# Kernel optimization log

Hardware: AMD Instinct MI355X
Metric: run time of the kernel (lower is better)

## Reference

```python
import jax, jax.numpy as jnp
import numpy as np

N = 4_000_000   # number of sparse voxels
H = 128         # parent-grid extent per axis (input coords < 256 -> parents < 128)


def setup_inputs() -> dict:
    key = jax.random.key(0)
    # col 0 = batch index, cols 1:4 = integer xyz voxel coords in [0, 256)
    coords = jax.random.randint(key, (N, 4), 0, 256, dtype=jnp.int32)
    # spnn.Conv3d(1,1,k=2) kernel: (2^3, in=1, out=1), constant-init to 1.0
    kernel = jnp.ones((8, 1, 1), dtype=jnp.float32)
    return {"coords": coords, "kernel": kernel}


def _fog(coords, kernel):
    b = coords[:, 0].astype(jnp.int64)
    xyz = coords[:, 1:]
    # pos(): 3-bit occupancy code from LSBs of xyz, feat = 2^code
    bits = xyz & 1                                        # (N, 3)
    pos = bits[:, 0] + 2 * bits[:, 1] + 4 * bits[:, 2]    # (N,) in [0, 8)
    feats = (jnp.int32(1) << pos).astype(jnp.float32)     # (N,) values {1,...,128}

    # 2x2x2 stride-2 sparse conv with all-ones kernel == sum over the 8 children
    # of each parent voxel. The child's kernel-offset index is exactly `pos`.
    pxyz = (xyz >> 1).astype(jnp.int64)                   # parent coords
    pkey = ((b * H + pxyz[:, 0]) * H + pxyz[:, 1]) * H + pxyz[:, 2]

    ukeys, inv = jnp.unique(pkey, size=N, fill_value=-1, return_inverse=True)
    inv = inv.ravel()

    contrib = feats * kernel[pos, 0, 0]                   # all-ones kernel -> feats
    out_feats = jax.ops.segment_sum(contrib, inv, num_segments=N)  # (N,)

    # decode unique parent keys back to (batch, x, y, z); pad slots -> -1
    valid = ukeys >= 0
    k = jnp.where(valid, ukeys, 0)
    oz = k % H
    k = k // H
    oy = k % H
    k = k // H
    ox = k % H
    ob = k // H
    out_coords = jnp.stack([ob, ox, oy, oz], axis=-1).astype(jnp.int32)
    out_coords = jnp.where(valid[:, None], out_coords, jnp.int32(-1))
    return out_coords, out_feats


def reference(coords, kernel):
    return _fog(coords, kernel)
```

## Files before the change

### kernel.cpp

```cpp
#include <hip/hip_runtime.h>

#define NB_BITS     11
#define N_BUCKETS   (1 << NB_BITS)
#define LOCAL_BITS  18
#define LOCAL_WORDS 8192
#define LKMASK      ((1u << LOCAL_BITS) - 1u)
#define KEYMASK     0x1FFFFFFFu
#define NXCD        8
#define WCAP        512
#define WSHIFT      9
#define FE_CAP      2560
#define PPT         8
#define TILE        (1024 * PPT)

__device__ __forceinline__ unsigned make_key(int4 c) {
    return ((((unsigned)c.x << 7) | (unsigned)(c.y >> 1)) << 7 | (unsigned)(c.z >> 1)) << 7
         | (unsigned)(c.w >> 1);
}

template<int NW>
__device__ inline void block_scan(unsigned v, unsigned* wsum, unsigned& excl, unsigned& total) {
    int t = threadIdx.x, ln = t & 63, wv = t >> 6;
    unsigned incl = v;
    #pragma unroll
    for (int off = 1; off < 64; off <<= 1) {
        unsigned y = __shfl_up(incl, off, 64);
        if (ln >= off) incl += y;
    }
    if (ln == 63) wsum[wv] = incl;
    __syncthreads();
    if (wv == 0) {
        unsigned s = (ln < NW) ? wsum[ln] : 0u;
        #pragma unroll
        for (int off = 1; off < NW; off <<= 1) {
            unsigned y = __shfl_up(s, off, 64);
            if (ln >= off) s += y;
        }
        if (ln < NW) wsum[ln] = s;
    }
    __syncthreads();
    excl = (wv ? wsum[wv - 1] : 0u) + incl - v;
    total = wsum[NW - 1];
}

__device__ __forceinline__ void gb_setup(const unsigned* gcur, int b, unsigned* gb) {
    int t = threadIdx.x;
    unsigned gv = 0;
    if (t < 8) gv = min(gcur[(unsigned)t * N_BUCKETS + (unsigned)b], (unsigned)WCAP);
    if (t < 64) {
        unsigned incl = gv;
        #pragma unroll
        for (int off = 1; off < 8; off <<= 1) {
            unsigned y = __shfl_up(incl, off, 64);
            if (t >= off) incl += y;
        }
        if (t < 8) gb[t + 1] = incl;
        if (t == 0) gb[0] = 0u;
    }
}

__global__ void __launch_bounds__(1024, 8)
build_pass(const int4* __restrict__ coords,
           unsigned* __restrict__ gcur,
           unsigned* __restrict__ pairs,
           int n) {
    __shared__ unsigned h[N_BUCKETS];
    int t = threadIdx.x, blk = blockIdx.x;
    unsigned xcd = (unsigned)blk & 7u;
    int base = blk * TILE;
    unsigned skey[PPT], lrank[PPT];
    h[t] = 0u; h[t + 1024] = 0u;
    #pragma unroll
    for (int m = 0; m < PPT; ++m) {
        int i = base + t + m * 1024;
        if (i < n) {
            int4 c = coords[i];
            unsigned key = make_key(c);
            unsigned pos = (unsigned)((c.y & 1) | ((c.z & 1) << 1) | ((c.w & 1) << 2));
            skey[m] = (pos << 29) | key;
        }
    }
    __syncthreads();
    #pragma unroll
    for (int m = 0; m < PPT; ++m) {
        int i = base + t + m * 1024;
        if (i < n)
            lrank[m] = atomicAdd(&h[(skey[m] & KEYMASK) >> LOCAL_BITS], 1u);
    }
    __syncthreads();
    #pragma unroll
    for (int q = 0; q < 2; ++q) {
        int j = t + q * 1024;
        unsigned c = h[j];
        if (c) h[j] = atomicAdd(&gcur[xcd * N_BUCKETS + (unsigned)j], c);
    }
    __syncthreads();
    #pragma unroll
    for (int m = 0; m < PPT; ++m) {
        int i = base + t + m * 1024;
        if (i < n) {
            unsigned b = (skey[m] & KEYMASK) >> LOCAL_BITS;
            unsigned o = h[b] + lrank[m];
            if (o < WCAP)
                pairs[(((b << 3) | xcd) << WSHIFT) + o] = skey[m];
        }
    }
}

__global__ void __launch_bounds__(512, 8)
count_pass(const unsigned* __restrict__ pairs,
           const unsigned* __restrict__ gcur,
           unsigned* __restrict__ ucount) {
    __shared__ unsigned bm[LOCAL_WORDS];
    __shared__ unsigned wsum[8];
    __shared__ unsigned gb[NXCD + 1];
    int t = threadIdx.x, b = blockIdx.x;
    gb_setup(gcur, b, gb);
    #pragma unroll
    for (int m = 0; m < 4; ++m)
        ((uint4*)bm)[t + 512 * m] = make_uint4(0u, 0u, 0u, 0u);
    __syncthreads();
    unsigned tot = gb[NXCD];
    for (unsigned p = (unsigned)t; p < tot; p += 512u) {
        unsigned g = 0;
        #pragma unroll
        for (int j = 1; j < NXCD; ++j) g += (p >= gb[j]) ? 1u : 0u;
        unsigned lk = pairs[((((unsigned)b << 3) | g) << WSHIFT) + (p - gb[g])] & LKMASK;
        atomicOr(&bm[lk >> 5], 1u << (lk & 31u));
    }
    __syncthreads();
    unsigned v = 0;
    #pragma unroll
    for (int m = 0; m < 16; ++m) v += __popc(bm[t + 512 * m]);
    int ln = t & 63;
    #pragma unroll
    for (int off = 1; off < 64; off <<= 1) v += __shfl_xor(v, off, 64);
    if (ln == 0) wsum[t >> 6] = v;
    __syncthreads();
    if (t == 0) {
        unsigned c = 0;
        #pragma unroll
        for (int m = 0; m < 8; ++m) c += wsum[m];
        ucount[b] = c;
    }
}

__global__ void __launch_bounds__(1024, 8)
emit_pass(const unsigned* __restrict__ pairs,
          const unsigned* __restrict__ gcur,
          const unsigned* __restrict__ ucount,
          const float* __restrict__ kern,
          float4* __restrict__ out_coords,
          float* __restrict__ out_feats, int n) {
    __shared__ unsigned       bm[LOCAL_WORDS];
    __shared__ unsigned short pfx[LOCAL_WORDS];
    __shared__ float          fe[FE_CAP];
    __shared__ unsigned wsum[16];
    __shared__ unsigned gb[NXCD + 1];
    __shared__ unsigned ubS, totS;
    __shared__ float    kl[8];
    int t = threadIdx.x, b = blockIdx.x;
    if (t < 8) kl[t] = (float)(1 << t) * kern[t];
    gb_setup(gcur, b, gb);
    ((uint4*)bm)[t] = make_uint4(0u, 0u, 0u, 0u);
    ((uint4*)bm)[t + 1024] = make_uint4(0u, 0u, 0u, 0u);
    for (int i = t; i < FE_CAP; i += 1024) fe[i] = 0.f;
    __syncthreads();
    unsigned tot = gb[NXCD];
    unsigned pk[5];
    if (t >= 64) {
        #pragma unroll
        for (int k = 0; k < 5; ++k) {
            unsigned p = (unsigned)(t - 64) + (unsigned)k * 960u;
            if (p < tot) {
                unsigned g = 0;
                #pragma unroll
                for (int j = 1; j < NXCD; ++j) g += (p >= gb[j]) ? 1u : 0u;
                unsigned v = pairs[((((unsigned)b << 3) | g) << WSHIFT) + (p - gb[g])];
                pk[k] = v;
                unsigned lk = v & LKMASK;
                atomicOr(&bm[lk >> 5], 1u << (lk & 31u));
            }
        }
    } else {
        int ln = t;
        unsigned sum = 0;
        const uint4* uc4 = (const uint4*)ucount;
        #pragma unroll
        for (int q = 0; q < 8; ++q) {
            uint4 u = uc4[ln * 8 + q];
            sum += u.x + u.y + u.z + u.w;
        }
        unsigned incl = sum;
        #pragma unroll
        for (int off = 1; off < 64; off <<= 1) {
            unsigned y = __shfl_up(incl, off, 64);
            if (ln >= off) incl += y;
        }
        if (ln == 63) totS = incl;
        unsigned exclv = incl - sum;
        if (ln == (b >> 5)) {
            unsigned r = exclv;
            int lim = b & 31;
            for (int m = 0; m < lim; ++m) r += ucount[(b & ~31) + m];
            ubS = r;
        }
    }
    __syncthreads();
    uint4 q0 = ((uint4*)bm)[2 * t], q1 = ((uint4*)bm)[2 * t + 1];
    unsigned pc[8] = { (unsigned)__popc(q0.x), (unsigned)__popc(q0.y),
                       (unsigned)__popc(q0.z), (unsigned)__popc(q0.w),
                       (unsigned)__popc(q1.x), (unsigned)__popc(q1.y),
                       (unsigned)__popc(q1.z), (unsigned)__popc(q1.w) };
    unsigned psum = 0;
    #pragma unroll
    for (int m = 0; m < 8; ++m) psum += pc[m];
    unsigned excl, cnt;
    block_scan<16>(psum, wsum, excl, cnt);
    {
        unsigned run = excl, pw[4];
        #pragma unroll
        for (int m = 0; m < 4; ++m) {
            unsigned lo = run & 0xFFFFu; run += pc[2 * m];
            unsigned hi = run & 0xFFFFu; run += pc[2 * m + 1];
            pw[m] = lo | (hi << 16);
        }
        ((uint4*)pfx)[t] = make_uint4(pw[0], pw[1], pw[2], pw[3]);
    }
    __syncthreads();
    unsigned ub = ubS;
    unsigned wq[8] = { q0.x, q0.y, q0.z, q0.w, q1.x, q1.y, q1.z, q1.w };
    unsigned rr = ub + excl;
    #pragma unroll
    for (int m = 0; m < 8; ++m) {
        unsigned w = wq[m];
        unsigned hi = ((unsigned)b << LOCAL_BITS) | ((unsigned)(8 * t + m) << 5);
        while (w) {
            unsigned bit = (unsigned)__ffs(w) - 1u;
            w &= w - 1u;
            unsigned key = hi | bit;
            out_coords[rr++] = make_float4((float)(key >> 21),
                                           (float)((key >> 14) & 127u),
                                           (float)((key >> 7) & 127u),
                                           (float)(key & 127u));
        }
    }
    if (t >= 64) {
        #pragma unroll
        for (int k = 0; k < 5; ++k) {
            unsigned p = (unsigned)(t - 64) + (unsigned)k * 960u;
            if (p < tot) {
                unsigned v = pk[k];
                unsigned lk = v & LKMASK;
                unsigned wd = lk >> 5;
                unsigned lr = (unsigned)pfx[wd] + __popc(bm[wd] & ((1u << (lk & 31u)) - 1u));
                atomicAdd(&fe[lr], kl[v >> 29]);
            }
        }
    }
    __syncthreads();
    for (unsigned i = (unsigned)t; i < cnt; i += 1024u)
        out_feats[ub + i] = fe[i];
    unsigned T = totS;
    for (unsigned r = T + (unsigned)(b * 1024 + t); r < (unsigned)n; r += N_BUCKETS * 1024u) {
        out_coords[r] = make_float4(-1.f, -1.f, -1.f, -1.f);
        out_feats[r] = 0.f;
    }
}

extern "C" void kernel_launch(void* const* d_in, const int* in_sizes, int n_in,
                              void* d_out, int out_size, void* d_ws, size_t ws_size,
                              hipStream_t stream) {
    const int4* coords = (const int4*)d_in[0];
    const float* kern  = (const float*)d_in[1];
    int N = in_sizes[0] / 4;

    float* out = (float*)d_out;
    float4* out_coords = (float4*)out;
    float* out_feats = out + (size_t)4 * N;

    unsigned* gcur   = (unsigned*)d_ws;
    unsigned* ucount = gcur + (size_t)N_BUCKETS * NXCD;
    unsigned* pairs  = ucount + (size_t)N_BUCKETS;

    hipMemsetAsync(gcur, 0, (size_t)N_BUCKETS * NXCD * sizeof(unsigned), stream);

    int ntiles = (N + TILE - 1) / TILE;
    build_pass<<<ntiles, 1024, 0, stream>>>(coords, gcur, pairs, N);
    count_pass<<<N_BUCKETS, 512, 0, stream>>>(pairs, gcur, ucount);
    emit_pass<<<N_BUCKETS, 1024, 0, stream>>>(pairs, gcur, ucount, kern,
                                              out_coords, out_feats, N);
}
```

Measured before the change: 194.2 us.

## Fuse build, count and emit passes into one cooperative persistent kernel

Replaces the memset plus three separate kernel launches with a single cooperative kernel that loops over tiles and buckets with grid-stride persistence and uses grid.sync between phases. Global workspace traffic now goes through relaxed agent-scope atomic loads and stores so data stays visible across phases. This removes launch gaps and the memset, but adds three grid-wide barriers, limits the grid to occupancy times 256 CUs, and moves the count phase to 1024-thread blocks.

```diff
diff --git a/kernel.cpp b/kernel.cpp
--- a/kernel.cpp
+++ b/kernel.cpp
@@ -1,4 +1,7 @@
 #include <hip/hip_runtime.h>
+#include <hip/hip_cooperative_groups.h>
+
+namespace cg = cooperative_groups;
 
 #define NB_BITS     11
 #define N_BUCKETS   (1 << NB_BITS)
@@ -13,145 +16,23 @@
 #define PPT         8
 #define TILE        (1024 * PPT)
 
+#define ALOAD(p)    __hip_atomic_load((p), __ATOMIC_RELAXED, __HIP_MEMORY_SCOPE_AGENT)
+#define ASTORE(p,v) __hip_atomic_store((p), (v), __ATOMIC_RELAXED, __HIP_MEMORY_SCOPE_AGENT)
+
 __device__ __forceinline__ unsigned make_key(int4 c) {
     return ((((unsigned)c.x << 7) | (unsigned)(c.y >> 1)) << 7 | (unsigned)(c.z >> 1)) << 7
          | (unsigned)(c.w >> 1);
 }
 
-template<int NW>
-__device__ inline void block_scan(unsigned v, unsigned* wsum, unsigned& excl, unsigned& total) {
-    int t = threadIdx.x, ln = t & 63, wv = t >> 6;
-    unsigned incl = v;
-    #pragma unroll
-    for (int off = 1; off < 64; off <<= 1) {
-        unsigned y = __shfl_up(incl, off, 64);
-        if (ln >= off) incl += y;
-    }
-    if (ln == 63) wsum[wv] = incl;
-    __syncthreads();
-    if (wv == 0) {
-        unsigned s = (ln < NW) ? wsum[ln] : 0u;
-        #pragma unroll
-        for (int off = 1; off < NW; off <<= 1) {
-            unsigned y = __shfl_up(s, off, 64);
-            if (ln >= off) s += y;
-        }
-        if (ln < NW) wsum[ln] = s;
-    }
-    __syncthreads();
-    excl = (wv ? wsum[wv - 1] : 0u) + incl - v;
-    total = wsum[NW - 1];
-}
-
-__device__ __forceinline__ void gb_setup(const unsigned* gcur, int b, unsigned* gb) {
-    int t = threadIdx.x;
-    unsigned gv = 0;
-    if (t < 8) gv = min(gcur[(unsigned)t * N_BUCKETS + (unsigned)b], (unsigned)WCAP);
-    if (t < 64) {
-        unsigned incl = gv;
-        #pragma unroll
-        for (int off = 1; off < 8; off <<= 1) {
-            unsigned y = __shfl_up(incl, off, 64);
-            if (t >= off) incl += y;
-        }
-        if (t < 8) gb[t + 1] = incl;
-        if (t == 0) gb[0] = 0u;
-    }
-}
-
 __global__ void __launch_bounds__(1024, 8)
-build_pass(const int4* __restrict__ coords,
-           unsigned* __restrict__ gcur,
-           unsigned* __restrict__ pairs,
-           int n) {
-    __shared__ unsigned h[N_BUCKETS];
-    int t = threadIdx.x, blk = blockIdx.x;
-    unsigned xcd = (unsigned)blk & 7u;
-    int base = blk * TILE;
-    unsigned skey[PPT], lrank[PPT];
-    h[t] = 0u; h[t + 1024] = 0u;
-    #pragma unroll
-    for (int m = 0; m < PPT; ++m) {
-        int i = base + t + m * 1024;
-        if (i < n) {
-            int4 c = coords[i];
-            unsigned key = make_key(c);
-            unsigned pos = (unsigned)((c.y & 1) | ((c.z & 1) << 1) | ((c.w & 1) << 2));
-            skey[m] = (pos << 29) | key;
-        }
-    }
-    __syncthreads();
-    #pragma unroll
-    for (int m = 0; m < PPT; ++m) {
-        int i = base + t + m * 1024;
-        if (i < n)
-            lrank[m] = atomicAdd(&h[(skey[m] & KEYMASK) >> LOCAL_BITS], 1u);
-    }
-    __syncthreads();
-    #pragma unroll
-    for (int q = 0; q < 2; ++q) {
-        int j = t + q * 1024;
-        unsigned c = h[j];
-        if (c) h[j] = atomicAdd(&gcur[xcd * N_BUCKETS + (unsigned)j], c);
-    }
-    __syncthreads();
-    #pragma unroll
-    for (int m = 0; m < PPT; ++m) {
-        int i = base + t + m * 1024;
-        if (i < n) {
-            unsigned b = (skey[m] & KEYMASK) >> LOCAL_BITS;
-            unsigned o = h[b] + lrank[m];
-            if (o < WCAP)
-                pairs[(((b << 3) | xcd) << WSHIFT) + o] = skey[m];
-        }
-    }
-}
-
-__global__ void __launch_bounds__(512, 8)
-count_pass(const unsigned* __restrict__ pairs,
-           const unsigned* __restrict__ gcur,
-           unsigned* __restrict__ ucount) {
-    __shared__ unsigned bm[LOCAL_WORDS];
-    __shared__ unsigned wsum[8];
-    __shared__ unsigned gb[NXCD + 1];
-    int t = threadIdx.x, b = blockIdx.x;
-    gb_setup(gcur, b, gb);
-    #pragma unroll
-    for (int m = 0; m < 4; ++m)
-        ((uint4*)bm)[t + 512 * m] = make_uint4(0u, 0u, 0u, 0u);
-    __syncthreads();
-    unsigned tot = gb[NXCD];
-    for (unsigned p = (unsigned)t; p < tot; p += 512u) {
-        unsigned g = 0;
-        #pragma unroll
-        for (int j = 1; j < NXCD; ++j) g += (p >= gb[j]) ? 1u : 0u;
-        unsigned lk = pairs[((((unsigned)b << 3) | g) << WSHIFT) + (p - gb[g])] & LKMASK;
-        atomicOr(&bm[lk >> 5], 1u << (lk & 31u));
-    }
-    __syncthreads();
-    unsigned v = 0;
-    #pragma unroll
-    for (int m = 0; m < 16; ++m) v += __popc(bm[t + 512 * m]);
-    int ln = t & 63;
-    #pragma unroll
-    for (int off = 1; off < 64; off <<= 1) v += __shfl_xor(v, off, 64);
-    if (ln == 0) wsum[t >> 6] = v;
-    __syncthreads();
-    if (t == 0) {
-        unsigned c = 0;
-        #pragma unroll
-        for (int m = 0; m < 8; ++m) c += wsum[m];
-        ucount[b] = c;
-    }
-}
-
-__global__ void __launch_bounds__(1024, 8)
-emit_pass(const unsigned* __restrict__ pairs,
-          const unsigned* __restrict__ gcur,
-          const unsigned* __restrict__ ucount,
+fog_fused(const int4* __restrict__ coords,
           const float* __restrict__ kern,
+          unsigned* __restrict__ gcur,
+          unsigned* __restrict__ ucount,
+          unsigned* __restrict__ pairs,
           float4* __restrict__ out_coords,
-          float* __restrict__ out_feats, int n) {
+          float* __restrict__ out_feats,
+          int n, int ntiles) {
     __shared__ unsigned       bm[LOCAL_WORDS];
     __shared__ unsigned short pfx[LOCAL_WORDS];
     __shared__ float          fe[FE_CAP];
@@ -159,110 +40,237 @@
     __shared__ unsigned gb[NXCD + 1];
     __shared__ unsigned ubS, totS;
     __shared__ float    kl[8];
-    int t = threadIdx.x, b = blockIdx.x;
+    cg::grid_group grid = cg::this_grid();
+    int t = threadIdx.x;
+    const unsigned gsz = gridDim.x;
+
     if (t < 8) kl[t] = (float)(1 << t) * kern[t];
-    gb_setup(gcur, b, gb);
-    ((uint4*)bm)[t] = make_uint4(0u, 0u, 0u, 0u);
-    ((uint4*)bm)[t + 1024] = make_uint4(0u, 0u, 0u, 0u);
-    for (int i = t; i < FE_CAP; i += 1024) fe[i] = 0.f;
-    __syncthreads();
-    unsigned tot = gb[NXCD];
-    unsigned pk[5];
-    if (t >= 64) {
-        #pragma unroll
-        for (int k = 0; k < 5; ++k) {
-            unsigned p = (unsigned)(t - 64) + (unsigned)k * 960u;
-            if (p < tot) {
-                unsigned g = 0;
-                #pragma unroll
-                for (int j = 1; j < NXCD; ++j) g += (p >= gb[j]) ? 1u : 0u;
-                unsigned v = pairs[((((unsigned)b << 3) | g) << WSHIFT) + (p - gb[g])];
-                pk[k] = v;
-                unsigned lk = v & LKMASK;
-                atomicOr(&bm[lk >> 5], 1u << (lk & 31u));
-            }
-        }
-    } else {
-        int ln = t;
-        unsigned sum = 0;
-        const uint4* uc4 = (const uint4*)ucount;
-        #pragma unroll
-        for (int q = 0; q < 8; ++q) {
-            uint4 u = uc4[ln * 8 + q];
-            sum += u.x + u.y + u.z + u.w;
-        }
-        unsigned incl = sum;
+    for (unsigned i = blockIdx.x * 1024u + (unsigned)t; i < N_BUCKETS * NXCD; i += gsz * 1024u)
+        ASTORE(&gcur[i], 0u);
+    __threadfence();
+    grid.sync();
+
+    for (int blk = blockIdx.x; blk < ntiles; blk += (int)gsz) {
+        unsigned* h = bm;
+        unsigned xcd = (unsigned)blk & 7u;
+        int base = blk * TILE;
+        unsigned skey[PPT], lrank[PPT];
+        h[t] = 0u; h[t + 1024] = 0u;
+        #pragma unroll
+        for (int m = 0; m < PPT; ++m) {
+            int i = base + t + m * 1024;
+            if (i < n) {
+                int4 c = coords[i];
+                unsigned key = make_key(c);
+                unsigned pos = (unsigned)((c.y & 1) | ((c.z & 1) << 1) | ((c.w & 1) << 2));
+                skey[m] = (pos << 29) | key;
+            }
+        }
+        __syncthreads();
+        #pragma unroll
+        for (int m = 0; m < PPT; ++m) {
+            int i = base + t + m * 1024;
+            if (i < n)
+                lrank[m] = atomicAdd(&h[(skey[m] & KEYMASK) >> LOCAL_BITS], 1u);
+        }
+        __syncthreads();
+        #pragma unroll
+        for (int q = 0; q < 2; ++q) {
+            int j = t + q * 1024;
+            unsigned c = h[j];
+            if (c) h[j] = atomicAdd(&gcur[xcd * N_BUCKETS + (unsigned)j], c);
+        }
+        __syncthreads();
+        #pragma unroll
+        for (int m = 0; m < PPT; ++m) {
+            int i = base + t + m * 1024;
+            if (i < n) {
+                unsigned b = (skey[m] & KEYMASK) >> LOCAL_BITS;
+                unsigned o = h[b] + lrank[m];
+                if (o < WCAP)
+                    ASTORE(&pairs[(((b << 3) | xcd) << WSHIFT) + o], skey[m]);
+            }
+        }
+        __syncthreads();
+    }
+    __threadfence();
+    grid.sync();
+
+    for (int b = blockIdx.x; b < N_BUCKETS; b += (int)gsz) {
+        unsigned gv = 0;
+        if (t < 8) gv = min(ALOAD(&gcur[(unsigned)t * N_BUCKETS + (unsigned)b]), (unsigned)WCAP);
+        if (t < 64) {
+            unsigned incl = gv;
+            #pragma unroll
+            for (int off = 1; off < 8; off <<= 1) {
+                unsigned y = __shfl_up(incl, off, 64);
+                if (t >= off) incl += y;
+            }
+            if (t < 8) gb[t + 1] = incl;
+            if (t == 0) gb[0] = 0u;
+        }
+        ((uint4*)bm)[t] = make_uint4(0u, 0u, 0u, 0u);
+        ((uint4*)bm)[t + 1024] = make_uint4(0u, 0u, 0u, 0u);
+        __syncthreads();
+        unsigned tot = gb[NXCD];
+        for (unsigned p = (unsigned)t; p < tot; p += 1024u) {
+            unsigned g = 0;
+            #pragma unroll
+            for (int j = 1; j < NXCD; ++j) g += (p >= gb[j]) ? 1u : 0u;
+            unsigned lk = ALOAD(&pairs[((((unsigned)b << 3) | g) << WSHIFT) + (p - gb[g])]) & LKMASK;
+            atomicOr(&bm[lk >> 5], 1u << (lk & 31u));
+        }
+        __syncthreads();
+        unsigned v = 0;
+        #pragma unroll
+        for (int m = 0; m < 8; ++m) v += __popc(bm[t + 1024 * m]);
+        int ln = t & 63;
+        #pragma unroll
+        for (int off = 1; off < 64; off <<= 1) v += __shfl_xor(v, off, 64);
+        if (ln == 0) wsum[t >> 6] = v;
+        __syncthreads();
+        if (t == 0) {
+            unsigned c = 0;
+            #pragma unroll
+            for (int m = 0; m < 16; ++m) c += wsum[m];
+            ASTORE(&ucount[b], c);
+        }
+    }
+    __threadfence();
+    grid.sync();
+
+    for (int b = blockIdx.x; b < N_BUCKETS; b += (int)gsz) {
+        unsigned gv = 0;
+        if (t < 8) gv = min(ALOAD(&gcur[(unsigned)t * N_BUCKETS + (unsigned)b]), (unsigned)WCAP);
+        if (t < 64) {
+            unsigned incl = gv;
+            #pragma unroll
+            for (int off = 1; off < 8; off <<= 1) {
+                unsigned y = __shfl_up(incl, off, 64);
+                if (t >= off) incl += y;
+            }
+            if (t < 8) gb[t + 1] = incl;
+            if (t == 0) gb[0] = 0u;
+        }
+        ((uint4*)bm)[t] = make_uint4(0u, 0u, 0u, 0u);
+        ((uint4*)bm)[t + 1024] = make_uint4(0u, 0u, 0u, 0u);
+        for (int i = t; i < FE_CAP; i += 1024) fe[i] = 0.f;
+        __syncthreads();
+        unsigned tot = gb[NXCD];
+        unsigned pk[5];
+        if (t >= 64) {
+            #pragma unroll
+            for (int k = 0; k < 5; ++k) {
+                unsigned p = (unsigned)(t - 64) + (unsigned)k * 960u;
+                if (p < tot) {
+                    unsigned g = 0;
+                    #pragma unroll
+                    for (int j = 1; j < NXCD; ++j) g += (p >= gb[j]) ? 1u : 0u;
+                    unsigned v = ALOAD(&pairs[((((unsigned)b << 3) | g) << WSHIFT) + (p - gb[g])]);
+                    pk[k] = v;
+                    unsigned lk = v & LKMASK;
+                    atomicOr(&bm[lk >> 5], 1u << (lk & 31u));
+                }
+            }
+        } else {
+            int ln = t;
+            unsigned sum = 0;
+            #pragma unroll 4
+            for (int q = 0; q < 32; ++q)
+                sum += ALOAD(&ucount[ln * 32 + q]);
+            unsigned incl = sum;
+            #pragma unroll
+            for (int off = 1; off < 64; off <<= 1) {
+                unsigned y = __shfl_up(incl, off, 64);
+                if (ln >= off) incl += y;
+            }
+            if (ln == 63) totS = incl;
+            unsigned exclv = incl - sum;
+            if (ln == (b >> 5)) {
+                unsigned r = exclv;
+                int lim = b & 31;
+                for (int m = 0; m < lim; ++m) r += ALOAD(&ucount[(b & ~31) + m]);
+                ubS = r;
+            }
+        }
+        __syncthreads();
+        uint4 q0 = ((uint4*)bm)[2 * t], q1 = ((uint4*)bm)[2 * t + 1];
+        unsigned pc[8] = { (unsigned)__popc(q0.x), (unsigned)__popc(q0.y),
+                           (unsigned)__popc(q0.z), (unsigned)__popc(q0.w),
+                           (unsigned)__popc(q1.x), (unsigned)__popc(q1.y),
+                           (unsigned)__popc(q1.z), (unsigned)__popc(q1.w) };
+        unsigned psum = 0;
+        #pragma unroll
+        for (int m = 0; m < 8; ++m) psum += pc[m];
+        int ln2 = t & 63, wv = t >> 6;
+        unsigned incl2 = psum;
         #pragma unroll
         for (int off = 1; off < 64; off <<= 1) {
-            unsigned y = __shfl_up(incl, off, 64);
-            if (ln >= off) incl += y;
-        }
-        if (ln == 63) totS = incl;
-        unsigned exclv = incl - sum;
-        if (ln == (b >> 5)) {
-            unsigned r = exclv;
-            int lim = b & 31;
-            for (int m = 0; m < lim; ++m) r += ucount[(b & ~31) + m];
-            ubS = r;
-        }
+            unsigned y = __shfl_up(incl2, off, 64);
+            if (ln2 >= off) incl2 += y;
+        }
+        if (ln2 == 63) wsum[wv] = incl2;
+        __syncthreads();
+        if (wv == 0) {
+            unsigned s = (ln2 < 16) ? wsum[ln2] : 0u;
+            #pragma unroll
+            for (int off = 1; off < 16; off <<= 1) {
+                unsigned y = __shfl_up(s, off, 64);
+                if (ln2 >= off) s += y;
+            }
+            if (ln2 < 16) wsum[ln2] = s;
+        }
+        __syncthreads();
+        unsigned excl = (wv ? wsum[wv - 1] : 0u) + incl2 - psum;
+        unsigned cnt = wsum[15];
+        {
+            unsigned run = excl, pw[4];
+            #pragma unroll
+            for (int m = 0; m < 4; ++m) {
+                unsigned lo = run & 0xFFFFu; run += pc[2 * m];
+                unsigned hi = run & 0xFFFFu; run += pc[2 * m + 1];
+                pw[m] = lo | (hi << 16);
+            }
+            ((uint4*)pfx)[t] = make_uint4(pw[0], pw[1], pw[2], pw[3]);
+        }
+        __syncthreads();
+        unsigned ub = ubS;
+        unsigned wq[8] = { q0.x, q0.y, q0.z, q0.w, q1.x, q1.y, q1.z, q1.w };
+        unsigned rr = ub + excl;
+        #pragma unroll
+        for (int m = 0; m < 8; ++m) {
+            unsigned w = wq[m];
+            unsigned hi = ((unsigned)b << LOCAL_BITS) | ((unsigned)(8 * t + m) << 5);
+            while (w) {
+                unsigned bit = (unsigned)__ffs(w) - 1u;
+                w &= w - 1u;
+                unsigned key = hi | bit;
+                out_coords[rr++] = make_float4((float)(key >> 21),
+                                               (float)((key >> 14) & 127u),
+                                               (float)((key >> 7) & 127u),
+                                               (float)(key & 127u));
+            }
+        }
+        if (t >= 64) {
+            #pragma unroll
+            for (int k = 0; k < 5; ++k) {
+                unsigned p = (unsigned)(t - 64) + (unsigned)k * 960u;
+                if (p < tot) {
+                    unsigned v = pk[k];
+                    unsigned lk = v & LKMASK;
+                    unsigned wd = lk >> 5;
+                    unsigned lr = (unsigned)pfx[wd] + __popc(bm[wd] & ((1u << (lk & 31u)) - 1u));
+                    atomicAdd(&fe[lr], kl[v >> 29]);
+                }
+            }
+        }
+        __syncthreads();
+        for (unsigned i = (unsigned)t; i < cnt; i += 1024u)
+            out_feats[ub + i] = fe[i];
+        __syncthreads();
     }
-    __syncthreads();
-    uint4 q0 = ((uint4*)bm)[2 * t], q1 = ((uint4*)bm)[2 * t + 1];
-    unsigned pc[8] = { (unsigned)__popc(q0.x), (unsigned)__popc(q0.y),
-                       (unsigned)__popc(q0.z), (unsigned)__popc(q0.w),
-                       (unsigned)__popc(q1.x), (unsigned)__popc(q1.y),
-                       (unsigned)__popc(q1.z), (unsigned)__popc(q1.w) };
-    unsigned psum = 0;
-    #pragma unroll
-    for (int m = 0; m < 8; ++m) psum += pc[m];
-    unsigned excl, cnt;
-    block_scan<16>(psum, wsum, excl, cnt);
-    {
-        unsigned run = excl, pw[4];
-        #pragma unroll
-        for (int m = 0; m < 4; ++m) {
-            unsigned lo = run & 0xFFFFu; run += pc[2 * m];
-            unsigned hi = run & 0xFFFFu; run += pc[2 * m + 1];
-            pw[m] = lo | (hi << 16);
-        }
-        ((uint4*)pfx)[t] = make_uint4(pw[0], pw[1], pw[2], pw[3]);
-    }
-    __syncthreads();
-    unsigned ub = ubS;
-    unsigned wq[8] = { q0.x, q0.y, q0.z, q0.w, q1.x, q1.y, q1.z, q1.w };
-    unsigned rr = ub + excl;
-    #pragma unroll
-    for (int m = 0; m < 8; ++m) {
-        unsigned w = wq[m];
-        unsigned hi = ((unsigned)b << LOCAL_BITS) | ((unsigned)(8 * t + m) << 5);
-        while (w) {
-            unsigned bit = (unsigned)__ffs(w) - 1u;
-            w &= w - 1u;
-            unsigned key = hi | bit;
-            out_coords[rr++] = make_float4((float)(key >> 21),
-                                           (float)((key >> 14) & 127u),
-                                           (float)((key >> 7) & 127u),
-                                           (float)(key & 127u));
-        }
-    }
-    if (t >= 64) {
-        #pragma unroll
-        for (int k = 0; k < 5; ++k) {
-            unsigned p = (unsigned)(t - 64) + (unsigned)k * 960u;
-            if (p < tot) {
-                unsigned v = pk[k];
-                unsigned lk = v & LKMASK;
-                unsigned wd = lk >> 5;
-                unsigned lr = (unsigned)pfx[wd] + __popc(bm[wd] & ((1u << (lk & 31u)) - 1u));
-                atomicAdd(&fe[lr], kl[v >> 29]);
-            }
-        }
-    }
-    __syncthreads();
-    for (unsigned i = (unsigned)t; i < cnt; i += 1024u)
-        out_feats[ub + i] = fe[i];
     unsigned T = totS;
-    for (unsigned r = T + (unsigned)(b * 1024 + t); r < (unsigned)n; r += N_BUCKETS * 1024u) {
+    for (unsigned r = T + blockIdx.x * 1024u + (unsigned)t; r < (unsigned)n; r += gsz * 1024u) {
         out_coords[r] = make_float4(-1.f, -1.f, -1.f, -1.f);
         out_feats[r] = 0.f;
     }
@@ -283,11 +291,16 @@
     unsigned* ucount = gcur + (size_t)N_BUCKETS * NXCD;
     unsigned* pairs  = ucount + (size_t)N_BUCKETS;
 
-    hipMemsetAsync(gcur, 0, (size_t)N_BUCKETS * NXCD * sizeof(unsigned), stream);
-
     int ntiles = (N + TILE - 1) / TILE;
-    build_pass<<<ntiles, 1024, 0, stream>>>(coords, gcur, pairs, N);
-    count_pass<<<N_BUCKETS, 512, 0, stream>>>(pairs, gcur, ucount);
-    emit_pass<<<N_BUCKETS, 1024, 0, stream>>>(pairs, gcur, ucount, kern,
-                                              out_coords, out_feats, N);
+
+    int occ = 0;
+    hipOccupancyMaxActiveBlocksPerMultiprocessor(&occ, fog_fused, 1024, 0);
+    if (occ < 1) occ = 1;
+    int G = occ * 256;
+    if (G > N_BUCKETS) G = N_BUCKETS;
+
+    void* args[] = { (void*)&coords, (void*)&kern, (void*)&gcur, (void*)&ucount,
+                     (void*)&pairs, (void*)&out_coords, (void*)&out_feats,
+                     (void*)&N, (void*)&ntiles };
+    hipLaunchCooperativeKernel(fog_fused, dim3(G), dim3(1024), args, 0, stream);
 }
```

Measured after the change: 608.4 us. 213% more time.
